# Performance work log

Measured on AMD Instinct MI355X. Metric: run time of the kernel, lower is better.

Reference implementation:

```python
import jax, jax.numpy as jnp
import numpy as np

UNITS = 1024
NUM_HEADS = 8


def setup_inputs() -> dict:
    key = jax.random.key(0)
    k1, k2, k3 = jax.random.split(key, 3)
    B, S = 8, 1024
    memory = jax.random.normal(k1, (B, S, 2 * UNITS), dtype=jnp.float32)
    query = jax.random.normal(k2, (B, S, UNITS), dtype=jnp.float32)
    seq_mask = jax.random.randint(k3, (B, S), 0, 2, dtype=jnp.int32)
    b = jnp.zeros((1,), dtype=jnp.float32)  # learned scalar bias added to logits
    return {"memory": memory, "query": query, "seq_mask": seq_mask, "b": b}


def _split_heads(x, n):
    # [B, S, D] -> [B, n, S, D//n]
    B, S, D = x.shape
    return x.reshape(B, S, n, D // n).transpose(0, 2, 1, 3)


def reference(memory, query, seq_mask, b):
    H = NUM_HEADS
    depth = UNITS // H
    Q = _split_heads(query, H) * (depth ** -0.5)          # [B,H,S,d]
    k_mem, v_mem = jnp.split(memory, 2, axis=2)
    K = _split_heads(k_mem, H)                            # [B,H,S,d]
    V = _split_heads(v_mem, H)                            # [B,H,S,d]
    logits = jnp.einsum('bhqd,bhkd->bhqk', Q, K) + b[0]   # [B,H,S,S]
    mask = seq_mask.astype(jnp.float32)[:, None, None, :]  # [B,1,1,S]
    logits = logits + (-1e30) * (1.0 - mask)
    weights = jax.nn.softmax(logits, axis=-1)
    out = jnp.einsum('bhqk,bhkd->bhqd', weights, V)       # [B,H,S,d]
    B, _, S, _ = out.shape
    return out.transpose(0, 2, 1, 3).reshape(B, S, UNITS)
```

## Files before the change

kernel.cpp:

```cpp
#include <hip/hip_runtime.h>
#include <stdint.h>


typedef __attribute__((ext_vector_type(8))) short bf16x8;
typedef __attribute__((ext_vector_type(4))) float f32x4;
typedef __attribute__((ext_vector_type(16))) float f32x16;
typedef __attribute__((ext_vector_type(4))) unsigned int u32x4;

#define NB 8
#define SS 1024
#define NH 8
#define DH 128
#define BM 128
#define BN 64
#define KPAD 136
#define VPAD 72

__device__ __forceinline__ unsigned short f2bf(float f) {
    unsigned int u = __builtin_bit_cast(unsigned int, f);
    u += 0x7fffu + ((u >> 16) & 1u);
    return (unsigned short)(u >> 16);
}

__device__ __forceinline__ unsigned int cvt_pk_bf16(float lo, float hi) {
#if __has_builtin(__builtin_amdgcn_cvt_pk_bf16_f32)
    typedef __attribute__((ext_vector_type(2))) __bf16 bf16x2_t;
    bf16x2_t r = __builtin_amdgcn_cvt_pk_bf16_f32(lo, hi);
    return __builtin_bit_cast(unsigned int, r);
#else
    return (unsigned int)f2bf(lo) | ((unsigned int)f2bf(hi) << 16);
#endif
}

__device__ __forceinline__ void bar_lgkm() {
    asm volatile("s_waitcnt lgkmcnt(0)" ::: "memory");
    __builtin_amdgcn_s_barrier();
    asm volatile("" ::: "memory");
}

__device__ __forceinline__ void pswap(unsigned int &a, unsigned int &b) {
#if __has_builtin(__builtin_amdgcn_permlane32_swap)
    auto r = __builtin_amdgcn_permlane32_swap(a, b, false, false);
    a = (unsigned int)r[0];
    b = (unsigned int)r[1];
#else
    unsigned int sa = (unsigned int)__shfl_xor((int)a, 32, 64);
    unsigned int sb = (unsigned int)__shfl_xor((int)b, 32, 64);
    const bool hh = (threadIdx.x & 32) != 0;
    unsigned int na = hh ? sb : a;
    unsigned int nb = hh ? b : sa;
    a = na; b = nb;
#endif
}

__global__ __launch_bounds__(256, 2)
void attn_flash(const float* __restrict__ mem,
                const float* __restrict__ query,
                const int* __restrict__ seq_mask,
                float* __restrict__ out)
{
    __shared__ unsigned short K_lds[BN * KPAD];
    __shared__ unsigned short Vt_lds[DH * VPAD];

    const int tid  = threadIdx.x;
    const int wave = tid >> 6;
    const int lane = tid & 63;
    const int hi   = lane >> 5;
    const int l31  = lane & 31;

    const int bh = blockIdx.x;
    const int b  = bh >> 3;
    const int h  = bh & 7;
    const int q0w = blockIdx.y * BM + wave * 32;

    bf16x8 qf[8];
    {
        const float* qb = query + ((size_t)(b * SS + q0w + l31) << 10) + h * DH + hi * 8;
        #pragma unroll
        for (int dep = 0; dep < 8; ++dep) {
            f32x4 lo = *(const f32x4*)(qb + dep * 16);
            f32x4 ho = *(const f32x4*)(qb + dep * 16 + 4);
            u32x4 q;
            q[0] = cvt_pk_bf16(lo[0], lo[1]);
            q[1] = cvt_pk_bf16(lo[2], lo[3]);
            q[2] = cvt_pk_bf16(ho[0], ho[1]);
            q[3] = cvt_pk_bf16(ho[2], ho[3]);
            qf[dep] = __builtin_bit_cast(bf16x8, q);
        }
    }

    f32x16 acc[4];
    #pragma unroll
    for (int dt = 0; dt < 4; ++dt)
        #pragma unroll
        for (int i = 0; i < 16; ++i) acc[dt][i] = 0.f;
    float l_i = 0.f;

    const float cs = 0.12752789747141537f;

    const int krow = tid >> 4;
    const int kcc  = (tid & 15) * 8;
    const int vq   = tid & 31;
    const int vg8  = tid >> 5;

    const float* kbase = mem + ((size_t)(b * SS) << 11) + h * DH;
    const float* vbase = kbase + 1024;
    const int* mbase = seq_mask + b * SS;

    f32x4 pka[4], pkb[4];
    f32x4 pva0[2], pva1[2], pvb0[2], pvb1[2];

    #pragma unroll
    for (int it = 0; it < 4; ++it) {
        const float* src = kbase + ((size_t)(it * 16 + krow) << 11) + kcc;
        pka[it] = *(const f32x4*)src;
        pkb[it] = *(const f32x4*)(src + 4);
    }
    #pragma unroll
    for (int task = 0; task < 2; ++task) {
        int d0 = vg8 * 8 + task * 64;
        const float* pa = vbase + ((size_t)(2 * vq) << 11) + d0;
        pva0[task] = *(const f32x4*)pa;
        pva1[task] = *(const f32x4*)(pa + 4);
        pvb0[task] = *(const f32x4*)(pa + 2048);
        pvb1[task] = *(const f32x4*)(pa + 2048 + 4);
    }

    for (int kt = 0; kt < SS / BN; ++kt) {
        const int kk0 = kt * BN;

        const int mv = mbase[kk0 + lane];

        bar_lgkm();

        #pragma unroll
        for (int it = 0; it < 4; ++it) {
            u32x4 t;
            t[0] = cvt_pk_bf16(pka[it][0], pka[it][1]);
            t[1] = cvt_pk_bf16(pka[it][2], pka[it][3]);
            t[2] = cvt_pk_bf16(pkb[it][0], pkb[it][1]);
            t[3] = cvt_pk_bf16(pkb[it][2], pkb[it][3]);
            *(u32x4*)&K_lds[(it * 16 + krow) * KPAD + kcc] = t;
        }
        #pragma unroll
        for (int task = 0; task < 2; ++task) {
            int d0 = vg8 * 8 + task * 64;
            #pragma unroll
            for (int j = 0; j < 8; ++j) {
                float av = (j < 4) ? pva0[task][j] : pva1[task][j - 4];
                float bv = (j < 4) ? pvb0[task][j] : pvb1[task][j - 4];
                *(unsigned int*)&Vt_lds[(d0 + j) * VPAD + 2 * vq] =
                    cvt_pk_bf16(av, bv);
            }
        }

        const int kkn = (kt < SS / BN - 1) ? kk0 + BN : kk0;
        #pragma unroll
        for (int it = 0; it < 4; ++it) {
            const float* src = kbase + ((size_t)(kkn + it * 16 + krow) << 11) + kcc;
            pka[it] = *(const f32x4*)src;
            pkb[it] = *(const f32x4*)(src + 4);
        }
        #pragma unroll
        for (int task = 0; task < 2; ++task) {
            int d0 = vg8 * 8 + task * 64;
            const float* pa = vbase + ((size_t)(kkn + 2 * vq) << 11) + d0;
            pva0[task] = *(const f32x4*)pa;
            pva1[task] = *(const f32x4*)(pa + 4);
            pvb0[task] = *(const f32x4*)(pa + 2048);
            pvb1[task] = *(const f32x4*)(pa + 2048 + 4);
        }

        const unsigned long long bmask = __ballot(mv != 0);
        const unsigned int wsh0 = (unsigned int)(bmask >> (4 * hi));
        const unsigned int wsh1 = (unsigned int)(bmask >> (32 + 4 * hi));

        bar_lgkm();

        #pragma unroll
        for (int jt = 0; jt < 2; ++jt) {
            const unsigned int mword = jt ? wsh1 : wsh0;

            f32x16 s;
            #pragma unroll
            for (int i = 0; i < 16; ++i) s[i] = 0.f;
            __builtin_amdgcn_s_setprio(1);
            #pragma unroll
            for (int dep = 0; dep < 8; ++dep) {
                bf16x8 kf = *(const bf16x8*)&K_lds[(jt * 32 + l31) * KPAD + dep * 16 + hi * 8];
                s = __builtin_amdgcn_mfma_f32_32x32x16_bf16(kf, qf[dep], s, 0, 0, 0);
            }
            __builtin_amdgcn_s_setprio(0);

            float p[16];
            #pragma unroll
            for (int r = 0; r < 16; ++r) {
                const int sr = (r & 3) + 8 * (r >> 2);
                float e = __builtin_amdgcn_exp2f(s[r] * cs);
                float m = (float)((mword >> sr) & 1u);
                p[r] = e * m;
            }
            {
                float t0 = (p[0] + p[1]) + (p[2] + p[3]);
                float t1 = (p[4] + p[5]) + (p[6] + p[7]);
                float t2 = (p[8] + p[9]) + (p[10] + p[11]);
                float t3 = (p[12] + p[13]) + (p[14] + p[15]);
                l_i += (t0 + t1) + (t2 + t3);
            }

            unsigned int w[8];
            #pragma unroll
            for (int i = 0; i < 8; ++i) w[i] = cvt_pk_bf16(p[2 * i], p[2 * i + 1]);
            pswap(w[0], w[2]); pswap(w[1], w[3]);
            pswap(w[4], w[6]); pswap(w[5], w[7]);
            bf16x8 af0 = __builtin_bit_cast(bf16x8, (u32x4){w[0], w[1], w[2], w[3]});
            bf16x8 af1 = __builtin_bit_cast(bf16x8, (u32x4){w[4], w[5], w[6], w[7]});

            __builtin_amdgcn_s_setprio(1);
            #pragma unroll
            for (int ksl = 0; ksl < 2; ++ksl) {
                bf16x8 ap = ksl ? af1 : af0;
                #pragma unroll
                for (int dt = 0; dt < 4; ++dt) {
                    bf16x8 bv = *(const bf16x8*)&Vt_lds[(dt * 32 + l31) * VPAD +
                                                        jt * 32 + ksl * 16 + hi * 8];
                    acc[dt] = __builtin_amdgcn_mfma_f32_32x32x16_bf16(ap, bv, acc[dt], 0, 0, 0);
                }
            }
            __builtin_amdgcn_s_setprio(0);
        }
    }

    float lt = l_i + __shfl_xor(l_i, 32, 64);
    float invl = 1.f / lt;
    #pragma unroll
    for (int r = 0; r < 16; ++r) {
        const int qrow = (r & 3) + 8 * (r >> 2) + 4 * hi;
        float iv = __shfl(invl, qrow, 64);
        float* ob = out + ((size_t)(b * SS + q0w + qrow) << 10) + h * DH + l31;
        #pragma unroll
        for (int dt = 0; dt < 4; ++dt)
            ob[dt * 32] = acc[dt][r] * iv;
    }
}

extern "C" void kernel_launch(void* const* d_in, const int* in_sizes, int n_in,
                              void* d_out, int out_size, void* d_ws, size_t ws_size,
                              hipStream_t stream)
{
    (void)in_sizes; (void)n_in; (void)d_ws; (void)ws_size; (void)out_size;
    const float* mem    = (const float*)d_in[0];
    const float* query  = (const float*)d_in[1];
    const int* seq_mask = (const int*)d_in[2];
    dim3 grid(NB * NH, SS / BM);
    attn_flash<<<grid, 256, 0, stream>>>(mem, query, seq_mask, (float*)d_out);
}
```

Before: 174.2 us.

## Double-buffer K/V tiles in LDS to drop one barrier per iteration

Switches K and transposed-V shared-memory tiles to a two-slot ring. The next tile is converted and stored into the alternate buffer after computing on the current one, so each key tile needs one barrier instead of two and the stores can overlap other waves' MFMA work. LDS use doubles to about 70 KB per block, which may limit occupancy at two blocks per CU, and the mask value is now carried a tile ahead.

After: 176.2 us. Within noise of the previous version (+1.1%).

```diff
diff --git a/kernel.cpp b/kernel.cpp
--- a/kernel.cpp
+++ b/kernel.cpp
@@ -15,6 +15,7 @@
 #define BN 64
 #define KPAD 136
 #define VPAD 72
+#define NT (SS / BN)
 
 __device__ __forceinline__ unsigned short f2bf(float f) {
     unsigned int u = __builtin_bit_cast(unsigned int, f);
@@ -59,8 +60,8 @@
                 const int* __restrict__ seq_mask,
                 float* __restrict__ out)
 {
-    __shared__ unsigned short K_lds[BN * KPAD];
-    __shared__ unsigned short Vt_lds[DH * VPAD];
+    __shared__ unsigned short K_lds[2][BN * KPAD];
+    __shared__ unsigned short Vt_lds[2][DH * VPAD];
 
     const int tid  = threadIdx.x;
     const int wave = tid >> 6;
@@ -109,6 +110,7 @@
 
     f32x4 pka[4], pkb[4];
     f32x4 pva0[2], pva1[2], pvb0[2], pvb1[2];
+    int pmv, pmv_next;
 
     #pragma unroll
     for (int it = 0; it < 4; ++it) {
@@ -125,58 +127,57 @@
         pvb0[task] = *(const f32x4*)(pa + 2048);
         pvb1[task] = *(const f32x4*)(pa + 2048 + 4);
     }
-
-    for (int kt = 0; kt < SS / BN; ++kt) {
-        const int kk0 = kt * BN;
-
-        const int mv = mbase[kk0 + lane];
-
-        bar_lgkm();
-
-        #pragma unroll
-        for (int it = 0; it < 4; ++it) {
-            u32x4 t;
-            t[0] = cvt_pk_bf16(pka[it][0], pka[it][1]);
-            t[1] = cvt_pk_bf16(pka[it][2], pka[it][3]);
-            t[2] = cvt_pk_bf16(pkb[it][0], pkb[it][1]);
-            t[3] = cvt_pk_bf16(pkb[it][2], pkb[it][3]);
-            *(u32x4*)&K_lds[(it * 16 + krow) * KPAD + kcc] = t;
+    pmv = mbase[lane];
+
+    #pragma unroll
+    for (int it = 0; it < 4; ++it) {
+        u32x4 t;
+        t[0] = cvt_pk_bf16(pka[it][0], pka[it][1]);
+        t[1] = cvt_pk_bf16(pka[it][2], pka[it][3]);
+        t[2] = cvt_pk_bf16(pkb[it][0], pkb[it][1]);
+        t[3] = cvt_pk_bf16(pkb[it][2], pkb[it][3]);
+        *(u32x4*)&K_lds[0][(it * 16 + krow) * KPAD + kcc] = t;
+    }
+    #pragma unroll
+    for (int task = 0; task < 2; ++task) {
+        int d0 = vg8 * 8 + task * 64;
+        #pragma unroll
+        for (int j = 0; j < 8; ++j) {
+            float av = (j < 4) ? pva0[task][j] : pva1[task][j - 4];
+            float bv = (j < 4) ? pvb0[task][j] : pvb1[task][j - 4];
+            *(unsigned int*)&Vt_lds[0][(d0 + j) * VPAD + 2 * vq] =
+                cvt_pk_bf16(av, bv);
         }
-        #pragma unroll
-        for (int task = 0; task < 2; ++task) {
-            int d0 = vg8 * 8 + task * 64;
-            #pragma unroll
-            for (int j = 0; j < 8; ++j) {
-                float av = (j < 4) ? pva0[task][j] : pva1[task][j - 4];
-                float bv = (j < 4) ? pvb0[task][j] : pvb1[task][j - 4];
-                *(unsigned int*)&Vt_lds[(d0 + j) * VPAD + 2 * vq] =
-                    cvt_pk_bf16(av, bv);
-            }
-        }
-
-        const int kkn = (kt < SS / BN - 1) ? kk0 + BN : kk0;
-        #pragma unroll
-        for (int it = 0; it < 4; ++it) {
-            const float* src = kbase + ((size_t)(kkn + it * 16 + krow) << 11) + kcc;
-            pka[it] = *(const f32x4*)src;
-            pkb[it] = *(const f32x4*)(src + 4);
-        }
-        #pragma unroll
-        for (int task = 0; task < 2; ++task) {
-            int d0 = vg8 * 8 + task * 64;
-            const float* pa = vbase + ((size_t)(kkn + 2 * vq) << 11) + d0;
-            pva0[task] = *(const f32x4*)pa;
-            pva1[task] = *(const f32x4*)(pa + 4);
-            pvb0[task] = *(const f32x4*)(pa + 2048);
-            pvb1[task] = *(const f32x4*)(pa + 2048 + 4);
-        }
-
-        const unsigned long long bmask = __ballot(mv != 0);
+    }
+
+    #pragma unroll
+    for (int it = 0; it < 4; ++it) {
+        const float* src = kbase + ((size_t)(BN + it * 16 + krow) << 11) + kcc;
+        pka[it] = *(const f32x4*)src;
+        pkb[it] = *(const f32x4*)(src + 4);
+    }
+    #pragma unroll
+    for (int task = 0; task < 2; ++task) {
+        int d0 = vg8 * 8 + task * 64;
+        const float* pa = vbase + ((size_t)(BN + 2 * vq) << 11) + d0;
+        pva0[task] = *(const f32x4*)pa;
+        pva1[task] = *(const f32x4*)(pa + 4);
+        pvb0[task] = *(const f32x4*)(pa + 2048);
+        pvb1[task] = *(const f32x4*)(pa + 2048 + 4);
+    }
+    pmv_next = mbase[BN + lane];
+
+    bar_lgkm();
+
+    for (int kt = 0; kt < NT; ++kt) {
+        const int cur = kt & 1;
+        const unsigned short* Kc = &K_lds[cur][0];
+        const unsigned short* Vc = &Vt_lds[cur][0];
+
+        const unsigned long long bmask = __ballot(pmv != 0);
         const unsigned int wsh0 = (unsigned int)(bmask >> (4 * hi));
         const unsigned int wsh1 = (unsigned int)(bmask >> (32 + 4 * hi));
 
-        bar_lgkm();
-
         #pragma unroll
         for (int jt = 0; jt < 2; ++jt) {
             const unsigned int mword = jt ? wsh1 : wsh0;
@@ -187,7 +188,7 @@
             __builtin_amdgcn_s_setprio(1);
             #pragma unroll
             for (int dep = 0; dep < 8; ++dep) {
-                bf16x8 kf = *(const bf16x8*)&K_lds[(jt * 32 + l31) * KPAD + dep * 16 + hi * 8];
+                bf16x8 kf = *(const bf16x8*)&Kc[(jt * 32 + l31) * KPAD + dep * 16 + hi * 8];
                 s = __builtin_amdgcn_mfma_f32_32x32x16_bf16(kf, qf[dep], s, 0, 0, 0);
             }
             __builtin_amdgcn_s_setprio(0);
@@ -222,12 +223,58 @@
                 bf16x8 ap = ksl ? af1 : af0;
                 #pragma unroll
                 for (int dt = 0; dt < 4; ++dt) {
-                    bf16x8 bv = *(const bf16x8*)&Vt_lds[(dt * 32 + l31) * VPAD +
-                                                        jt * 32 + ksl * 16 + hi * 8];
+                    bf16x8 bv = *(const bf16x8*)&Vc[(dt * 32 + l31) * VPAD +
+                                                    jt * 32 + ksl * 16 + hi * 8];
                     acc[dt] = __builtin_amdgcn_mfma_f32_32x32x16_bf16(ap, bv, acc[dt], 0, 0, 0);
                 }
             }
             __builtin_amdgcn_s_setprio(0);
+        }
+
+        if (kt < NT - 1) {
+            unsigned short* Kn = &K_lds[cur ^ 1][0];
+            unsigned short* Vn = &Vt_lds[cur ^ 1][0];
+            #pragma unroll
+            for (int it = 0; it < 4; ++it) {
+                u32x4 t;
+                t[0] = cvt_pk_bf16(pka[it][0], pka[it][1]);
+                t[1] = cvt_pk_bf16(pka[it][2], pka[it][3]);
+                t[2] = cvt_pk_bf16(pkb[it][0], pkb[it][1]);
+                t[3] = cvt_pk_bf16(pkb[it][2], pkb[it][3]);
+                *(u32x4*)&Kn[(it * 16 + krow) * KPAD + kcc] = t;
+            }
+            #pragma unroll
+            for (int task = 0; task < 2; ++task) {
+                int d0 = vg8 * 8 + task * 64;
+                #pragma unroll
+                for (int j = 0; j < 8; ++j) {
+                    float av = (j < 4) ? pva0[task][j] : pva1[task][j - 4];
+                    float bv = (j < 4) ? pvb0[task][j] : pvb1[task][j - 4];
+                    *(unsigned int*)&Vn[(d0 + j) * VPAD + 2 * vq] =
+                        cvt_pk_bf16(av, bv);
+                }
+            }
+
+            const int kk2 = (kt < NT - 2) ? (kt + 2) * BN : (kt + 1) * BN;
+            #pragma unroll
+            for (int it = 0; it < 4; ++it) {
+                const float* src = kbase + ((size_t)(kk2 + it * 16 + krow) << 11) + kcc;
+                pka[it] = *(const f32x4*)src;
+                pkb[it] = *(const f32x4*)(src + 4);
+            }
+            #pragma unroll
+            for (int task = 0; task < 2; ++task) {
+                int d0 = vg8 * 8 + task * 64;
+                const float* pa = vbase + ((size_t)(kk2 + 2 * vq) << 11) + d0;
+                pva0[task] = *(const f32x4*)pa;
+                pva1[task] = *(const f32x4*)(pa + 4);
+                pvb0[task] = *(const f32x4*)(pa + 2048);
+                pvb1[task] = *(const f32x4*)(pa + 2048 + 4);
+            }
+            pmv = pmv_next;
+            pmv_next = mbase[kk2 + lane];
+
+            bar_lgkm();
         }
     }
 
```
